# Kernel optimization log

Hardware: AMD Instinct MI355X
Metric: run time of the kernel (lower is better)

The kernel has to match this reference:

```python
import jax, jax.numpy as jnp
import numpy as np

DIM = 512
HEADS = 8
DHEAD = 64
INNER = HEADS * DHEAD
CHUNK = 8
GAMMA = 1.0
EPS = 1e-8
LN_EPS = 1e-5


def setup_inputs() -> dict:
    key = jax.random.key(0)
    ks = jax.random.split(key, 10)
    B, N = 64, 256
    return {
        "q": jax.random.normal(ks[0], (B, N, DIM), jnp.float32),
        "k": jax.random.normal(ks[1], (B, N, DIM), jnp.float32),
        "v": jax.random.normal(ks[2], (B, N, DIM), jnp.float32),
        "ln_gamma": jnp.ones((DIM,), jnp.float32),
        "ln_beta": jnp.zeros((DIM,), jnp.float32),
        "W_in": jax.random.normal(ks[3], (DIM, INNER), jnp.float32) / np.sqrt(DIM),
        "W_out": jax.random.normal(ks[4], (INNER, DIM), jnp.float32) / np.sqrt(INNER),
        "b_out": jnp.zeros((DIM,), jnp.float32),
        "cov_logit": jnp.asarray(0.6, jnp.float32),
        "var_logit": jnp.asarray(0.2, jnp.float32),
        "use_advanced": 1,
    }


def _layernorm(x, g, b):
    mu = jnp.mean(x, axis=-1, keepdims=True)
    var = jnp.mean(jnp.square(x - mu), axis=-1, keepdims=True)
    return (x - mu) * jax.lax.rsqrt(var + LN_EPS) * g + b


def _transform(t, ln_gamma, ln_beta, W_in):
    # [B,N,dim] -> [h,B,N,d]
    B, N, _ = t.shape
    f = _layernorm(t, ln_gamma, ln_beta) @ W_in
    return f.reshape(B, N, HEADS, DHEAD).transpose(2, 0, 1, 3)


def _chunk_stats(E):
    # E: [M, N, d], chunks of size CHUNK over M. Returns per-chunk scalars V, C of shape [M//CHUNK].
    M, N, d = E.shape
    nc = M // CHUNK
    Ec = E.reshape(nc, CHUNK, N, d)
    # variance component: torch.var is unbiased (ddof=1) over seq dim
    sigma = jnp.sqrt(jnp.var(Ec, axis=2, ddof=1) + EPS)  # [nc, CHUNK, d]
    V = jnp.mean(jax.nn.relu(GAMMA - sigma), axis=(1, 2))  # [nc]
    # covariance component: per-sample off-diagonal energy, averaged per chunk
    centered = Ec - jnp.mean(Ec, axis=2, keepdims=True)
    cov = jnp.einsum("csni,csnj->csij", centered, centered) / (N - 1)  # [nc,CHUNK,d,d]
    total = jnp.sum(jnp.square(cov), axis=(2, 3))
    diag = jnp.sum(jnp.square(jnp.diagonal(cov, axis1=2, axis2=3)), axis=2)
    C = jnp.mean((total - diag) / d, axis=1)  # [nc]
    return V, C


def reference(q, k, v, ln_gamma, ln_beta, W_in, W_out, b_out, cov_logit, var_logit, use_advanced):
    f_q = _transform(q, ln_gamma, ln_beta, W_in)  # [h,B,N,d]
    f_k = _transform(k, ln_gamma, ln_beta, W_in)
    f_v = _transform(v, ln_gamma, ln_beta, W_in)
    h, B, N, d = f_q.shape

    # cosine similarity
    dots_qk = jnp.einsum("hbnd,hbmd->hbnm", f_q, f_k)
    qn = jnp.linalg.norm(f_q, axis=-1)  # [h,B,N]
    kn = jnp.linalg.norm(f_k, axis=-1)
    cosine_sim = dots_qk / (qn[..., :, None] * kn[..., None, :])

    if use_advanced:
        Vq, Cq = _chunk_stats(f_q.reshape(h * B, N, d))
        Vk, Ck = _chunk_stats(f_k.reshape(h * B, N, d))
        var_component = jnp.repeat(Vq * Vk, CHUNK).reshape(h, B, 1, 1)
        cov_component = jnp.repeat(Cq * Ck, CHUNK).reshape(h, B, 1, 1)
    else:
        qc = f_q - jnp.mean(f_q, axis=-1, keepdims=True)
        kc = f_k - jnp.mean(f_k, axis=-1, keepdims=True)
        cov_component = jnp.einsum("hbnd,hbmd->hbnm", qc, kc) / d
        q_var = jnp.var(f_q, axis=-1, ddof=1, keepdims=True)  # [h,B,N,1]
        k_var = jnp.var(f_k, axis=-1, ddof=1, keepdims=True)
        var_component = (q_var * jnp.swapaxes(k_var, -1, -2)) / d

    cov_w = jax.nn.sigmoid(cov_logit)
    var_w = jax.nn.sigmoid(var_logit)
    cos_w = 1.0 - cov_w - var_w
    dots = cos_w * cosine_sim + cov_w * cov_component + var_w * var_component
    out = jnp.einsum("hbnm,hbmd->hbnd", dots, f_v)
    out = out.transpose(1, 2, 0, 3).reshape(B, N, h * d)
    return out @ W_out + b_out
```

## Files before the change

kernel.cpp:

```cpp
#include <hip/hip_runtime.h>
#include <cstdint>
#include <cstddef>

#define DIM    512
#define HEADS  8
#define DHEAD  64
#define NSEQ   256
#define BATCH  64
#define NROWS  (BATCH * NSEQ)
#define HB     (HEADS * BATCH)

typedef unsigned short u16;
typedef __bf16 bf16x8 __attribute__((ext_vector_type(8)));
typedef float  f32x4  __attribute__((ext_vector_type(4)));

__device__ __forceinline__ float sigmoidf_(float x) { return 1.0f / (1.0f + expf(-x)); }

__device__ __forceinline__ u16 f2bf(float f) {
    union { float f; unsigned u; } a; a.f = f;
    return (u16)((a.u + 0x7fffu + ((a.u >> 16) & 1u)) >> 16);
}

__device__ __forceinline__ void gload16(const void* g, void* l) {
    __builtin_amdgcn_global_load_lds((const __attribute__((address_space(1))) void*)g,
                                     (__attribute__((address_space(3))) void*)l, 16, 0, 0);
}

__global__ __launch_bounds__(256)
void transpose_cast_kernel(const float* __restrict__ W0, const float* __restrict__ W1,
                           const float* __restrict__ gam, const float* __restrict__ bet,
                           u16* __restrict__ WT, float* __restrict__ cs,
                           float* __restrict__ bW)
{
    __shared__ float tile[64][65];
    const int t = threadIdx.x;
    const int bx = blockIdx.x * 64, by = blockIdx.y * 64;
    const int z = blockIdx.z;
    const float* W = z ? W1 : W0;
    u16* dst = WT + (size_t)z * 512 * 512;
#pragma unroll
    for (int i = 0; i < 16; ++i) {
        int idx = i * 256 + t, r = idx >> 6, c = idx & 63;
        tile[r][c] = W[(size_t)(by + r) * DIM + bx + c];
    }
    __syncthreads();
#pragma unroll
    for (int i = 0; i < 16; ++i) {
        int idx = i * 256 + t, r = idx >> 6, c = idx & 63;
        float wv = tile[c][r];
        if (!z) wv *= gam[by + c];
        dst[(size_t)(bx + r) * DIM + by + c] = f2bf(wv);
    }
    if (!z && t < 64) {
        float s1 = 0.f, s2 = 0.f;
#pragma unroll 8
        for (int r = 0; r < 64; ++r) {
            float wv = tile[r][t];
            s1 += gam[by + r] * wv;
            s2 += bet[by + r] * wv;
        }
        atomicAdd(cs + bx + t, s1);
        atomicAdd(bW + bx + t, s2);
    }
}

__global__ __launch_bounds__(256)
void in_gemm_kernel(const float* __restrict__ Xq, const float* __restrict__ Xk,
                    const float* __restrict__ Xv, const u16* __restrict__ BT,
                    const float* __restrict__ cs, const float* __restrict__ bW,
                    u16* __restrict__ FT, u16* __restrict__ Fseq)
{
    __shared__ __align__(16) u16 shm[128 * 136];
    __shared__ float muL[128], rsL[128];
    float* Asf = (float*)shm;
    u16*  Bs   = shm + 8192;
    u16*  Ct   = shm;
    const int t = threadIdx.x, lane = t & 63, w = t >> 6;
    const int wr = w >> 1, wc = w & 1;
    const int flat = blockIdx.y * 4 + blockIdx.x;
    const int rt = (flat & 7) * 48 + ((flat >> 3) >> 2);
    const int c0 = ((flat >> 3) & 3) * 128;
    const int r0 = rt * 128;
    const int cl = lane & 15, q = lane >> 4;
    const int tns = r0 >> 14, lr0 = r0 & 16383;
    const float* X = (tns == 0) ? Xq : (tns == 1) ? Xk : Xv;

    f32x4 acc[4][4];
#pragma unroll
    for (int i = 0; i < 4; ++i)
#pragma unroll
        for (int j = 0; j < 4; ++j) acc[i][j] = (f32x4){0.f, 0.f, 0.f, 0.f};
    float s1[4] = {0.f, 0.f, 0.f, 0.f}, s2[4] = {0.f, 0.f, 0.f, 0.f};

    for (int k0 = 0; k0 < DIM; k0 += 32) {
#pragma unroll
        for (int i = 0; i < 4; ++i) {
            int idx = i * 256 + t;
            int row = idx >> 3, chs = idx & 7;
            int chg = chs ^ (row & 7);
            gload16(X + (size_t)(lr0 + row) * DIM + k0 + chg * 4, (char*)shm + idx * 16);
        }
#pragma unroll
        for (int i = 0; i < 2; ++i) {
            int idx = i * 256 + t;
            int row = idx >> 2, ch = idx & 3;
            gload16(BT + (size_t)(c0 + row) * DIM + k0 + ch * 8, Bs + idx * 8);
        }
        __syncthreads();
        bf16x8 af[4], bfr[4];
#pragma unroll
        for (int mi = 0; mi < 4; ++mi) {
            int rl = wr * 64 + mi * 16 + cl;
            int slo = (2 * q) ^ (rl & 7);
            float4 fl = ((const float4*)Asf)[rl * 8 + slo];
            float4 fh = ((const float4*)Asf)[rl * 8 + (slo ^ 1)];
            if (wc == 0) {
                s1[mi] += (fl.x + fl.y) + (fl.z + fl.w) + (fh.x + fh.y) + (fh.z + fh.w);
                s2[mi] += fl.x * fl.x + fl.y * fl.y + fl.z * fl.z + fl.w * fl.w
                        + fh.x * fh.x + fh.y * fh.y + fh.z * fh.z + fh.w * fh.w;
            }
            af[mi][0] = (__bf16)fl.x; af[mi][1] = (__bf16)fl.y;
            af[mi][2] = (__bf16)fl.z; af[mi][3] = (__bf16)fl.w;
            af[mi][4] = (__bf16)fh.x; af[mi][5] = (__bf16)fh.y;
            af[mi][6] = (__bf16)fh.z; af[mi][7] = (__bf16)fh.w;
        }
#pragma unroll
        for (int ni = 0; ni < 4; ++ni)
            bfr[ni] = *(const bf16x8*)(Bs + (wc * 64 + ni * 16 + cl) * 32 + q * 8);
#pragma unroll
        for (int mi = 0; mi < 4; ++mi)
#pragma unroll
            for (int ni = 0; ni < 4; ++ni)
                acc[mi][ni] = __builtin_amdgcn_mfma_f32_16x16x32_bf16(af[mi], bfr[ni],
                                                                      acc[mi][ni], 0, 0, 0);
        __syncthreads();
    }

    if (wc == 0) {
#pragma unroll
        for (int mi = 0; mi < 4; ++mi) {
            float a = s1[mi], b = s2[mi];
            a += __shfl_xor(a, 16, 64); a += __shfl_xor(a, 32, 64);
            b += __shfl_xor(b, 16, 64); b += __shfl_xor(b, 32, 64);
            if (q == 0) {
                int rl = wr * 64 + mi * 16 + cl;
                float mu = a * (1.f / DIM);
                float var = b * (1.f / DIM) - mu * mu;
                muL[rl] = mu;
                rsL[rl] = rsqrtf(var + 1e-5f);
            }
        }
    }
    __syncthreads();

    {
        float csv[4], bwv[4];
#pragma unroll
        for (int ni = 0; ni < 4; ++ni) {
            int col = c0 + wc * 64 + ni * 16 + cl;
            csv[ni] = cs[col]; bwv[ni] = bW[col];
        }
#pragma unroll
        for (int mi = 0; mi < 4; ++mi)
#pragma unroll
            for (int r = 0; r < 4; ++r) {
                int rl = wr * 64 + mi * 16 + q * 4 + r;
                float mu = muL[rl], rs = rsL[rl];
#pragma unroll
                for (int ni = 0; ni < 4; ++ni)
                    acc[mi][ni][r] = rs * (acc[mi][ni][r] - mu * csv[ni]) + bwv[ni];
            }
    }

    const int b = (r0 >> 8) & 63, n0 = r0 & 255;

    if (tns == 0) {
#pragma unroll
        for (int mi = 0; mi < 4; ++mi) {
            int lrow = wr * 64 + mi * 16 + q * 4;
#pragma unroll
            for (int ni = 0; ni < 4; ++ni) {
                int lcol = wc * 64 + ni * 16 + cl;
#pragma unroll
                for (int r = 0; r < 4; ++r)
                    Ct[(lrow + r) * 136 + lcol] = f2bf(acc[mi][ni][r]);
            }
        }
        __syncthreads();
#pragma unroll
        for (int i = 0; i < 8; ++i) {
            int idx = t + 256 * i, row = idx >> 4, ch = idx & 15;
            *(uint4*)(Fseq + (size_t)(lr0 + row) * DIM + c0 + ch * 8) =
                *(const uint4*)(Ct + row * 136 + ch * 8);
        }
        __syncthreads();
    }
#pragma unroll
    for (int mi = 0; mi < 4; ++mi) {
        int lrow = wr * 64 + mi * 16 + q * 4;
#pragma unroll
        for (int ni = 0; ni < 4; ++ni) {
            int lcol = wc * 64 + ni * 16 + cl;
#pragma unroll
            for (int r = 0; r < 4; ++r)
                Ct[lcol * 136 + lrow + r] = f2bf(acc[mi][ni][r]);
        }
    }
    __syncthreads();
#pragma unroll
    for (int i = 0; i < 8; ++i) {
        int idx = t + 256 * i, lc = idx >> 4, ch = idx & 15;
        *(uint4*)(FT + (((size_t)(tns * 64 + b) * 512 + c0 + lc) * 256 + n0 + ch * 8)) =
            *(const uint4*)(Ct + lc * 136 + ch * 8);
    }
}

__global__ __launch_bounds__(256)
void stats_kernel(const u16* __restrict__ FT, float* __restrict__ norms,
                  float2* __restrict__ vc)
{
    __shared__ u16 ET[64 * 264];
    __shared__ float mu[64];
    __shared__ float red[4][64];
    __shared__ float wr3[4][3];
    const int hb = blockIdx.x, tns = blockIdx.y, h = hb >> 6, b = hb & 63;
    const int t = threadIdx.x, lane = t & 63, w = t >> 6, cl = lane & 15, q = lane >> 4;
    const size_t Fb = ((size_t)(tns * 64 + b) * 512 + h * 64) * 256;

#pragma unroll
    for (int i = 0; i < 8; ++i) {
        int idx = t + 256 * i;
        int row = idx >> 5, ch = idx & 31;
        *(bf16x8*)(ET + row * 264 + ch * 8) =
            *(const bf16x8*)(FT + Fb + (size_t)row * 256 + ch * 8);
    }
    __syncthreads();

    {
        float s = 0.f;
#pragma unroll
        for (int d = 0; d < 64; ++d) {
            float x = (float)*(const __bf16*)(ET + d * 264 + t);
            s += x * x;
        }
        norms[((size_t)tns * HB + hb) * 256 + t] = sqrtf(s);
    }
    {
        int d = t & 63, part = t >> 6;
        float s = 0.f;
#pragma unroll
        for (int i = 0; i < 8; ++i) {
            bf16x8 v8 = *(const bf16x8*)(ET + d * 264 + part * 64 + i * 8);
#pragma unroll
            for (int j = 0; j < 8; ++j) s += (float)v8[j];
        }
        red[part][d] = s;
    }
    __syncthreads();
    if (t < 64) mu[t] = (red[0][t] + red[1][t] + red[2][t] + red[3][t]) * (1.f / 256.f);
    __syncthreads();

    f32x4 g[4];
#pragma unroll
    for (int nj = 0; nj < 4; ++nj) g[nj] = (f32x4){0.f, 0.f, 0.f, 0.f};
#pragma unroll
    for (int ks = 0; ks < 8; ++ks) {
        bf16x8 af = *(const bf16x8*)(ET + (16 * w + cl) * 264 + ks * 32 + q * 8);
#pragma unroll
        for (int nj = 0; nj < 4; ++nj) {
            bf16x8 bfr = *(const bf16x8*)(ET + (16 * nj + cl) * 264 + ks * 32 + q * 8);
            g[nj] = __builtin_amdgcn_mfma_f32_16x16x32_bf16(af, bfr, g[nj], 0, 0, 0);
        }
    }
    float t2 = 0.f, d2 = 0.f, vs = 0.f;
#pragma unroll
    for (int nj = 0; nj < 4; ++nj) {
        int j = 16 * nj + cl;
        float mj = mu[j];
#pragma unroll
        for (int r = 0; r < 4; ++r) {
            int i = 16 * w + 4 * q + r;
            float gc = (g[nj][r] - 256.f * mu[i] * mj) * (1.f / 255.f);
            float g2 = gc * gc;
            t2 += g2;
            if (i == j) {
                d2 += g2;
                float sig = sqrtf(gc + 1e-8f);
                vs += fmaxf(1.f - sig, 0.f);
            }
        }
    }
#pragma unroll
    for (int o = 32; o > 0; o >>= 1) {
        t2 += __shfl_xor(t2, o, 64);
        d2 += __shfl_xor(d2, o, 64);
        vs += __shfl_xor(vs, o, 64);
    }
    if (lane == 0) { wr3[w][0] = t2; wr3[w][1] = d2; wr3[w][2] = vs; }
    __syncthreads();
    if (t == 0) {
        float T = 0.f, D = 0.f, V = 0.f;
        for (int i = 0; i < 4; ++i) { T += wr3[i][0]; D += wr3[i][1]; V += wr3[i][2]; }
        vc[(size_t)tns * HB + hb] = make_float2(V * (1.f / 64.f), (T - D) * (1.f / 64.f));
    }
}

__global__ __launch_bounds__(256)
void attn_kernel(const u16* __restrict__ FT, const u16* __restrict__ Fseq,
                 const float* __restrict__ norms, const float2* __restrict__ vc,
                 const float* __restrict__ cov_logit, const float* __restrict__ var_logit,
                 u16* __restrict__ G)
{
    __shared__ u16 pool[256 * 72];
    __shared__ u16 MT[64 * 72];
    __shared__ float invq[256], invk[256], sv[64];
    const int hb = blockIdx.x, h = hb >> 6, b = hb & 63;
    const int t = threadIdx.x, lane = t & 63, w = t >> 6, cl = lane & 15, q = lane >> 4;
    u16* KT = pool;
    u16* VT = pool + 64 * 136;

    const float cw = sigmoidf_(*cov_logit), vw = sigmoidf_(*var_logit);
    const float cosw = 1.f - cw - vw;
    float s_hb;
    {
        int basec = hb & ~7;
        float vq = 0, cq = 0, vk = 0, ck = 0;
#pragma unroll
        for (int m = 0; m < 8; ++m) {
            float2 a = vc[basec + m];       vq += a.x; cq += a.y;
            float2 bb = vc[HB + basec + m]; vk += bb.x; ck += bb.y;
        }
        s_hb = (cw * cq * ck + vw * vq * vk) * (1.f / 64.f);
    }

    invq[t] = 1.f / norms[((size_t)0 * HB + hb) * 256 + t];
    invk[t] = 1.f / norms[((size_t)1 * HB + hb) * 256 + t];
    __syncthreads();

    const size_t FTk = ((size_t)(1 * 64 + b) * 512 + h * 64) * 256;
    const size_t FTv = ((size_t)(2 * 64 + b) * 512 + h * 64) * 256;
    f32x4 acc1[4];
#pragma unroll
    for (int nj = 0; nj < 4; ++nj) acc1[nj] = (f32x4){0.f, 0.f, 0.f, 0.f};
    float sp[4] = {0.f, 0.f, 0.f, 0.f};

    for (int c = 0; c < 2; ++c) {
#pragma unroll
        for (int i = 0; i < 4; ++i) {
            int idx = t + 256 * i;
            int row = idx >> 4, ch = idx & 15;
            int n0 = c * 128 + ch * 8;
            bf16x8 kv = *(const bf16x8*)(FT + FTk + (size_t)row * 256 + n0);
            bf16x8 vv = *(const bf16x8*)(FT + FTv + (size_t)row * 256 + n0);
            bf16x8 ksc;
#pragma unroll
            for (int j = 0; j < 8; ++j) ksc[j] = (__bf16)((float)kv[j] * invk[n0 + j]);
            *(bf16x8*)(KT + row * 136 + ch * 8) = ksc;
            *(bf16x8*)(VT + row * 136 + ch * 8) = vv;
        }
        __syncthreads();
#pragma unroll
        for (int ks = 0; ks < 4; ++ks) {
            bf16x8 af = *(const bf16x8*)(KT + (16 * w + cl) * 136 + ks * 32 + q * 8);
#pragma unroll
            for (int nj = 0; nj < 4; ++nj) {
                bf16x8 bfr = *(const bf16x8*)(VT + (16 * nj + cl) * 136 + ks * 32 + q * 8);
                if (w == 0) {
                    float s = 0.f;
#pragma unroll
                    for (int j = 0; j < 8; ++j) s += (float)bfr[j];
                    sp[nj] += s;
                }
                acc1[nj] = __builtin_amdgcn_mfma_f32_16x16x32_bf16(af, bfr, acc1[nj], 0, 0, 0);
            }
        }
        __syncthreads();
    }
    if (w == 0) {
#pragma unroll
        for (int nj = 0; nj < 4; ++nj) {
            float s = sp[nj];
            s += __shfl_xor(s, 16, 64);
            s += __shfl_xor(s, 32, 64);
            if (q == 0) sv[16 * nj + cl] = s;
        }
    }
#pragma unroll
    for (int nj = 0; nj < 4; ++nj)
#pragma unroll
        for (int r = 0; r < 4; ++r)
            MT[(16 * nj + cl) * 72 + 16 * w + 4 * q + r] = f2bf(acc1[nj][r]);
    __syncthreads();

    f32x4 acc2[4][4];
#pragma unroll
    for (int mi = 0; mi < 4; ++mi)
#pragma unroll
        for (int nj = 0; nj < 4; ++nj) acc2[mi][nj] = (f32x4){0.f, 0.f, 0.f, 0.f};
    const size_t Fq = (size_t)(b * 256) * DIM + h * 64;
#pragma unroll
    for (int ks2 = 0; ks2 < 2; ++ks2) {
        bf16x8 bfm[4];
#pragma unroll
        for (int nj = 0; nj < 4; ++nj)
            bfm[nj] = *(const bf16x8*)(MT + (16 * nj + cl) * 72 + ks2 * 32 + q * 8);
#pragma unroll
        for (int mi = 0; mi < 4; ++mi) {
            bf16x8 aq = *(const bf16x8*)(Fseq + Fq +
                         (size_t)(64 * w + 16 * mi + cl) * DIM + ks2 * 32 + q * 8);
#pragma unroll
            for (int nj = 0; nj < 4; ++nj)
                acc2[mi][nj] = __builtin_amdgcn_mfma_f32_16x16x32_bf16(aq, bfm[nj],
                                                                       acc2[mi][nj], 0, 0, 0);
        }
    }
    __syncthreads();
    u16* Os = pool;
#pragma unroll
    for (int mi = 0; mi < 4; ++mi) {
        int nbase = 64 * w + 16 * mi + 4 * q;
#pragma unroll
        for (int nj = 0; nj < 4; ++nj) {
            int j = 16 * nj + cl;
            float svj = sv[j];
#pragma unroll
            for (int r = 0; r < 4; ++r) {
                float o = cosw * acc2[mi][nj][r] * invq[nbase + r] + s_hb * svj;
                Os[(nbase + r) * 72 + j] = f2bf(o);
            }
        }
    }
    __syncthreads();
#pragma unroll
    for (int i = 0; i < 8; ++i) {
        int cidx = t + 256 * i;
        int row = cidx >> 3, ch = cidx & 7;
        *(uint4*)(G + (size_t)(b * 256 + row) * DIM + h * 64 + ch * 8) =
            *(const uint4*)(Os + row * 72 + ch * 8);
    }
}

__global__ __launch_bounds__(256)
void out_gemm_kernel(const u16* __restrict__ A, const u16* __restrict__ BT,
                     const float* __restrict__ bias, float* __restrict__ C)
{
    __shared__ u16 As[128 * 32];
    __shared__ u16 Bs[128 * 32];
    const int t = threadIdx.x, lane = t & 63, w = t >> 6;
    const int wr = w >> 1, wc = w & 1;
    const int flat = blockIdx.y * 4 + blockIdx.x;
    const int rt = (flat & 7) * 16 + ((flat >> 3) >> 2);
    const int c0 = ((flat >> 3) & 3) * 128;
    const int r0 = rt * 128;
    const int cl = lane & 15, q = lane >> 4;

    f32x4 acc[4][4];
#pragma unroll
    for (int i = 0; i < 4; ++i)
#pragma unroll
        for (int j = 0; j < 4; ++j) acc[i][j] = (f32x4){0.f, 0.f, 0.f, 0.f};

    for (int k0 = 0; k0 < DIM; k0 += 32) {
#pragma unroll
        for (int i = 0; i < 2; ++i) {
            int idx = i * 256 + t;
            int row = idx >> 2, ch = idx & 3;
            gload16(A  + (size_t)(r0 + row) * DIM + k0 + ch * 8, As + idx * 8);
            gload16(BT + (size_t)(c0 + row) * DIM + k0 + ch * 8, Bs + idx * 8);
        }
        __syncthreads();
        bf16x8 af[4], bfr[4];
#pragma unroll
        for (int mi = 0; mi < 4; ++mi)
            af[mi] = *(const bf16x8*)(As + (wr * 64 + mi * 16 + cl) * 32 + q * 8);
#pragma unroll
        for (int ni = 0; ni < 4; ++ni)
            bfr[ni] = *(const bf16x8*)(Bs + (wc * 64 + ni * 16 + cl) * 32 + q * 8);
#pragma unroll
        for (int mi = 0; mi < 4; ++mi)
#pragma unroll
            for (int ni = 0; ni < 4; ++ni)
                acc[mi][ni] = __builtin_amdgcn_mfma_f32_16x16x32_bf16(af[mi], bfr[ni],
                                                                      acc[mi][ni], 0, 0, 0);
        __syncthreads();
    }
#pragma unroll
    for (int mi = 0; mi < 4; ++mi) {
        int row0 = r0 + wr * 64 + mi * 16 + q * 4;
#pragma unroll
        for (int ni = 0; ni < 4; ++ni) {
            int col = c0 + wc * 64 + ni * 16 + cl;
            float bv = bias[col];
#pragma unroll
            for (int r = 0; r < 4; ++r)
                C[(size_t)(row0 + r) * DIM + col] = acc[mi][ni][r] + bv;
        }
    }
}

extern "C" void kernel_launch(void* const* d_in, const int* in_sizes, int n_in,
                              void* d_out, int out_size, void* d_ws, size_t ws_size,
                              hipStream_t stream)
{
    const float* q         = (const float*)d_in[0];
    const float* k         = (const float*)d_in[1];
    const float* v         = (const float*)d_in[2];
    const float* ln_g      = (const float*)d_in[3];
    const float* ln_b      = (const float*)d_in[4];
    const float* W_in      = (const float*)d_in[5];
    const float* W_out     = (const float*)d_in[6];
    const float* b_out     = (const float*)d_in[7];
    const float* cov_logit = (const float*)d_in[8];
    const float* var_logit = (const float*)d_in[9];
    float* out = (float*)d_out;

    char* base = (char*)d_ws;
    u16*    FT    = (u16*)base;
    u16*    Fseq  = (u16*)(base + 50331648);
    u16*    Gb    = (u16*)(base + 67108864);
    u16*    WT    = (u16*)(base + 83886080);
    float*  norms = (float*)(base + 84934656);
    float2* vc    = (float2*)(base + 85983232);
    float*  cs    = (float*)(base + 85991424);
    float*  bW    = cs + 512;

    hipMemsetAsync(cs, 0, 4096, stream);
    transpose_cast_kernel<<<dim3(8, 8, 2), 256, 0, stream>>>(W_in, W_out, ln_g, ln_b,
                                                             WT, cs, bW);
    in_gemm_kernel<<<dim3(4, 3 * NROWS / 128), 256, 0, stream>>>(q, k, v, WT, cs, bW,
                                                                 FT, Fseq);
    stats_kernel<<<dim3(HB, 2), 256, 0, stream>>>(FT, norms, vc);
    attn_kernel<<<dim3(HB), 256, 0, stream>>>(FT, Fseq, norms, vc,
                                              cov_logit, var_logit, Gb);
    out_gemm_kernel<<<dim3(4, NROWS / 128), 256, 0, stream>>>(
        Gb, WT + 512 * 512, b_out, out);
}
```

Before: 259.3 us.

## Double-buffer input GEMM with register-staged bf16 conversion of A tile

The input projection GEMM now prefetches the next K-slice of X into registers and B via async LDS loads while MFMAs run on the current buffer. X is converted to bf16 once at staging time and stored in a swizzled bf16 LDS layout, so the per-wave float-to-bf16 conversion and the duplicated LN statistics work move to the staging threads. The two barriers per iteration drop to one. This costs extra registers for the prefetched float4s and adds a different swizzle and reduction pattern for the row statistics.

```diff
diff --git a/kernel.cpp b/kernel.cpp
--- a/kernel.cpp
+++ b/kernel.cpp
@@ -70,11 +70,9 @@
                     const float* __restrict__ cs, const float* __restrict__ bW,
                     u16* __restrict__ FT, u16* __restrict__ Fseq)
 {
-    __shared__ __align__(16) u16 shm[128 * 136];
+    __shared__ __align__(16) u16 shm[17408];
     __shared__ float muL[128], rsL[128];
-    float* Asf = (float*)shm;
-    u16*  Bs   = shm + 8192;
-    u16*  Ct   = shm;
+    u16* Ct = shm;
     const int t = threadIdx.x, lane = t & 63, w = t >> 6;
     const int wr = w >> 1, wc = w & 1;
     const int flat = blockIdx.y * 4 + blockIdx.x;
@@ -85,6 +83,11 @@
     const int tns = r0 >> 14, lr0 = r0 & 16383;
     const float* X = (tns == 0) ? Xq : (tns == 1) ? Xk : Xv;
 
+    const int sc = t & 7;
+    int srow[4];
+#pragma unroll
+    for (int i = 0; i < 4; ++i) srow[i] = (i * 256 + t) >> 3;
+
     f32x4 acc[4][4];
 #pragma unroll
     for (int i = 0; i < 4; ++i)
@@ -92,63 +95,90 @@
         for (int j = 0; j < 4; ++j) acc[i][j] = (f32x4){0.f, 0.f, 0.f, 0.f};
     float s1[4] = {0.f, 0.f, 0.f, 0.f}, s2[4] = {0.f, 0.f, 0.f, 0.f};
 
-    for (int k0 = 0; k0 < DIM; k0 += 32) {
-#pragma unroll
-        for (int i = 0; i < 4; ++i) {
-            int idx = i * 256 + t;
-            int row = idx >> 3, chs = idx & 7;
-            int chg = chs ^ (row & 7);
-            gload16(X + (size_t)(lr0 + row) * DIM + k0 + chg * 4, (char*)shm + idx * 16);
-        }
-#pragma unroll
-        for (int i = 0; i < 2; ++i) {
-            int idx = i * 256 + t;
-            int row = idx >> 2, ch = idx & 3;
-            gload16(BT + (size_t)(c0 + row) * DIM + k0 + ch * 8, Bs + idx * 8);
-        }
-        __syncthreads();
+    float4 nA[4];
+#pragma unroll
+    for (int i = 0; i < 4; ++i)
+        nA[i] = *(const float4*)(X + (size_t)(lr0 + srow[i]) * DIM + sc * 4);
+#pragma unroll
+    for (int i = 0; i < 2; ++i) {
+        int idx = i * 256 + t, row = idx >> 2, ch = idx & 3;
+        gload16(BT + (size_t)(c0 + row) * DIM + ch * 8, shm + 8192 + idx * 8);
+    }
+#pragma unroll
+    for (int i = 0; i < 4; ++i) {
+        float4 f = nA[i];
+        s1[i] += (f.x + f.y) + (f.z + f.w);
+        s2[i] += f.x * f.x + f.y * f.y + f.z * f.z + f.w * f.w;
+        int row = srow[i];
+        int off = row * 32 + (((((sc >> 1) ^ ((row >> 1) & 3)) << 1) | (sc & 1)) << 2);
+        union { __bf16 h[4]; uint2 u; } p;
+        p.h[0] = (__bf16)f.x; p.h[1] = (__bf16)f.y;
+        p.h[2] = (__bf16)f.z; p.h[3] = (__bf16)f.w;
+        *(uint2*)(shm + off) = p.u;
+    }
+    __syncthreads();
+
+    for (int ks = 0; ks < 16; ++ks) {
+        const int cur = ks & 1;
+        u16* Ab = shm + cur * 4096;
+        u16* Bb = shm + 8192 + cur * 4096;
+        if (ks < 15) {
+            const int k1 = (ks + 1) * 32;
+#pragma unroll
+            for (int i = 0; i < 4; ++i)
+                nA[i] = *(const float4*)(X + (size_t)(lr0 + srow[i]) * DIM + k1 + sc * 4);
+#pragma unroll
+            for (int i = 0; i < 2; ++i) {
+                int idx = i * 256 + t, row = idx >> 2, ch = idx & 3;
+                gload16(BT + (size_t)(c0 + row) * DIM + k1 + ch * 8,
+                        shm + 8192 + (cur ^ 1) * 4096 + idx * 8);
+            }
+        }
         bf16x8 af[4], bfr[4];
 #pragma unroll
         for (int mi = 0; mi < 4; ++mi) {
             int rl = wr * 64 + mi * 16 + cl;
-            int slo = (2 * q) ^ (rl & 7);
-            float4 fl = ((const float4*)Asf)[rl * 8 + slo];
-            float4 fh = ((const float4*)Asf)[rl * 8 + (slo ^ 1)];
-            if (wc == 0) {
-                s1[mi] += (fl.x + fl.y) + (fl.z + fl.w) + (fh.x + fh.y) + (fh.z + fh.w);
-                s2[mi] += fl.x * fl.x + fl.y * fl.y + fl.z * fl.z + fl.w * fl.w
-                        + fh.x * fh.x + fh.y * fh.y + fh.z * fh.z + fh.w * fh.w;
-            }
-            af[mi][0] = (__bf16)fl.x; af[mi][1] = (__bf16)fl.y;
-            af[mi][2] = (__bf16)fl.z; af[mi][3] = (__bf16)fl.w;
-            af[mi][4] = (__bf16)fh.x; af[mi][5] = (__bf16)fh.y;
-            af[mi][6] = (__bf16)fh.z; af[mi][7] = (__bf16)fh.w;
+            af[mi] = *(const bf16x8*)(Ab + rl * 32 + (q ^ ((rl >> 1) & 3)) * 8);
         }
 #pragma unroll
         for (int ni = 0; ni < 4; ++ni)
-            bfr[ni] = *(const bf16x8*)(Bs + (wc * 64 + ni * 16 + cl) * 32 + q * 8);
+            bfr[ni] = *(const bf16x8*)(Bb + (wc * 64 + ni * 16 + cl) * 32 + q * 8);
 #pragma unroll
         for (int mi = 0; mi < 4; ++mi)
 #pragma unroll
             for (int ni = 0; ni < 4; ++ni)
                 acc[mi][ni] = __builtin_amdgcn_mfma_f32_16x16x32_bf16(af[mi], bfr[ni],
                                                                       acc[mi][ni], 0, 0, 0);
-        __syncthreads();
-    }
-
-    if (wc == 0) {
-#pragma unroll
-        for (int mi = 0; mi < 4; ++mi) {
-            float a = s1[mi], b = s2[mi];
-            a += __shfl_xor(a, 16, 64); a += __shfl_xor(a, 32, 64);
-            b += __shfl_xor(b, 16, 64); b += __shfl_xor(b, 32, 64);
-            if (q == 0) {
-                int rl = wr * 64 + mi * 16 + cl;
-                float mu = a * (1.f / DIM);
-                float var = b * (1.f / DIM) - mu * mu;
-                muL[rl] = mu;
-                rsL[rl] = rsqrtf(var + 1e-5f);
-            }
+        if (ks < 15) {
+            u16* An = shm + (cur ^ 1) * 4096;
+#pragma unroll
+            for (int i = 0; i < 4; ++i) {
+                float4 f = nA[i];
+                s1[i] += (f.x + f.y) + (f.z + f.w);
+                s2[i] += f.x * f.x + f.y * f.y + f.z * f.z + f.w * f.w;
+                int row = srow[i];
+                int off = row * 32 +
+                          (((((sc >> 1) ^ ((row >> 1) & 3)) << 1) | (sc & 1)) << 2);
+                union { __bf16 h[4]; uint2 u; } p;
+                p.h[0] = (__bf16)f.x; p.h[1] = (__bf16)f.y;
+                p.h[2] = (__bf16)f.z; p.h[3] = (__bf16)f.w;
+                *(uint2*)(An + off) = p.u;
+            }
+        }
+        __syncthreads();
+    }
+
+#pragma unroll
+    for (int i = 0; i < 4; ++i) {
+        float a = s1[i], b2 = s2[i];
+        a += __shfl_xor(a, 1, 64); a += __shfl_xor(a, 2, 64); a += __shfl_xor(a, 4, 64);
+        b2 += __shfl_xor(b2, 1, 64); b2 += __shfl_xor(b2, 2, 64); b2 += __shfl_xor(b2, 4, 64);
+        if (sc == 0) {
+            int row = srow[i];
+            float mu = a * (1.f / DIM);
+            float var = b2 * (1.f / DIM) - mu * mu;
+            muL[row] = mu;
+            rsL[row] = rsqrtf(var + 1e-5f);
         }
     }
     __syncthreads();
```

Result: slower. 309.9 us (+19.5%).
